# Kernel tuning notes

Measured on AMD Instinct MI355X. Metric: run time of the kernel, lower is better.

Reference implementation:

```python
import jax, jax.numpy as jnp
import numpy as np

D_MODEL = 1024
NUM_HEADS = 16
D_K = D_MODEL // NUM_HEADS
D_FF = 4096
B, S = 4, 2048
EPS = 1e-5


def _linear_params(key, d_in, d_out):
    # torch nn.Linear default init: U(-1/sqrt(d_in), 1/sqrt(d_in))
    k1, k2 = jax.random.split(key)
    bound = 1.0 / np.sqrt(d_in)
    W = jax.random.uniform(k1, (d_in, d_out), jnp.float32, -bound, bound)
    b = jax.random.uniform(k2, (d_out,), jnp.float32, -bound, bound)
    return W, b


def setup_inputs() -> dict:
    key = jax.random.key(0)
    ks = jax.random.split(key, 8)
    x = jax.random.normal(ks[0], (B, S, D_MODEL), jnp.float32)
    Wq, bq = _linear_params(ks[1], D_MODEL, D_MODEL)
    Wk, bk = _linear_params(ks[2], D_MODEL, D_MODEL)
    Wv, bv = _linear_params(ks[3], D_MODEL, D_MODEL)
    Wo, bo = _linear_params(ks[4], D_MODEL, D_MODEL)
    W1, b1 = _linear_params(ks[5], D_MODEL, D_FF)
    W2, b2 = _linear_params(ks[6], D_FF, D_MODEL)
    ln1_g = jnp.ones((D_MODEL,), jnp.float32)
    ln1_b = jnp.zeros((D_MODEL,), jnp.float32)
    ln2_g = jnp.ones((D_MODEL,), jnp.float32)
    ln2_b = jnp.zeros((D_MODEL,), jnp.float32)
    return dict(x=x, Wq=Wq, bq=bq, Wk=Wk, bk=bk, Wv=Wv, bv=bv, Wo=Wo, bo=bo,
                W1=W1, b1=b1, W2=W2, b2=b2,
                ln1_g=ln1_g, ln1_b=ln1_b, ln2_g=ln2_g, ln2_b=ln2_b)


def _layernorm(x, g, b):
    mu = jnp.mean(x, axis=-1, keepdims=True)
    var = jnp.mean(jnp.square(x - mu), axis=-1, keepdims=True)
    return (x - mu) * jax.lax.rsqrt(var + EPS) * g + b


def _attention(h, Wq, bq, Wk, bk, Wv, bv, Wo, bo):
    b, s, _ = h.shape
    def split_heads(t):  # (b,s,d) -> (b,H,s,dk)
        return t.reshape(b, s, NUM_HEADS, D_K).transpose(0, 2, 1, 3)
    Q = split_heads(h @ Wq + bq)
    K = split_heads(h @ Wk + bk)
    V = split_heads(h @ Wv + bv)
    scores = jnp.einsum('bhqd,bhkd->bhqk', Q, K) / np.sqrt(D_K)
    causal = jnp.tril(jnp.ones((s, s), dtype=bool))  # True = keep
    scores = jnp.where(causal, scores, -jnp.inf)
    attn = jax.nn.softmax(scores, axis=-1)
    out = jnp.einsum('bhqk,bhkd->bhqd', attn, V)
    out = out.transpose(0, 2, 1, 3).reshape(b, s, D_MODEL)
    return out @ Wo + bo


def reference(x, Wq, bq, Wk, bk, Wv, bv, Wo, bo, W1, b1, W2, b2,
              ln1_g, ln1_b, ln2_g, ln2_b):
    # pre-norm residual block
    x = x + _attention(_layernorm(x, ln1_g, ln1_b), Wq, bq, Wk, bk, Wv, bv, Wo, bo)
    h = _layernorm(x, ln2_g, ln2_b)
    x = x + (jax.nn.relu(h @ W1 + b1) @ W2 + b2)
    return x
```

## Files before the change

### kernel.cpp

```cpp
#include <hip/hip_runtime.h>
#include <hip/hip_bf16.h>

typedef __bf16 bf16;
typedef __attribute__((ext_vector_type(8))) __bf16 bf16x8;
typedef __attribute__((ext_vector_type(4))) float f32x4;

#define D_MODEL 1024
#define NHEADS  16
#define DK      64
#define DFF     4096
#define BATCH   4
#define SEQ     2048
#define NTOK    (BATCH*SEQ)
#define QSCALE  0.18033688011112042f

#if __has_builtin(__builtin_amdgcn_exp2f)
#define EXP2F(x) __builtin_amdgcn_exp2f(x)
#else
#define EXP2F(x) exp2f(x)
#endif

__device__ __forceinline__ void gload16(const bf16* g, bf16* l) {
    __builtin_amdgcn_global_load_lds((const __attribute__((address_space(1))) void*)g,
                                     (__attribute__((address_space(3))) void*)l, 16, 0, 0);
}

__global__ __launch_bounds__(256) void transpose_cast4(
    const float* __restrict__ W0, const float* __restrict__ W1,
    const float* __restrict__ W2, const float* __restrict__ W3,
    bf16* __restrict__ T0, bf16* __restrict__ T1,
    bf16* __restrict__ T2, bf16* __restrict__ T3)
{
    const int z = blockIdx.z;
    const float* W = (z == 0) ? W0 : (z == 1) ? W1 : (z == 2) ? W2 : W3;
    bf16*       Wt = (z == 0) ? T0 : (z == 1) ? T1 : (z == 2) ? T2 : T3;
    const int K = 1024, N = 1024;
    __shared__ float tile[32][33];
    const int tx = threadIdx.x, ty = threadIdx.y;
    const int n0 = blockIdx.x * 32, k0 = blockIdx.y * 32;
#pragma unroll
    for (int i = 0; i < 4; ++i)
        tile[ty + i*8][tx] = W[(size_t)(k0 + ty + i*8) * N + n0 + tx];
    __syncthreads();
#pragma unroll
    for (int i = 0; i < 4; ++i)
        Wt[(size_t)(n0 + ty + i*8) * K + k0 + tx] = (bf16)tile[tx][ty + i*8];
}

__global__ __launch_bounds__(256) void transpose_cast(
    const float* __restrict__ W, bf16* __restrict__ Wt, int K, int N)
{
    __shared__ float tile[32][33];
    const int tx = threadIdx.x, ty = threadIdx.y;
    const int n0 = blockIdx.x * 32, k0 = blockIdx.y * 32;
#pragma unroll
    for (int i = 0; i < 4; ++i)
        tile[ty + i*8][tx] = W[(size_t)(k0 + ty + i*8) * N + n0 + tx];
    __syncthreads();
#pragma unroll
    for (int i = 0; i < 4; ++i)
        Wt[(size_t)(n0 + ty + i*8) * K + k0 + tx] = (bf16)tile[tx][ty + i*8];
}

__global__ __launch_bounds__(256) void transpose_v(
    const bf16* __restrict__ V, bf16* __restrict__ VT)
{
    __shared__ bf16 t[64][72];
    const int bh = blockIdx.y;
    const int s0 = blockIdx.x * 64;
    const int r  = threadIdx.x >> 2;
    const int c0 = (threadIdx.x & 3) * 16;
    const bf16* Vb = V  + (size_t)bh * SEQ * DK;
    bf16*       Tb = VT + (size_t)bh * DK * SEQ;
#pragma unroll
    for (int i = 0; i < 2; ++i) {
        bf16x8 v = *(const bf16x8*)&Vb[(size_t)(s0 + r) * DK + c0 + i*8];
#pragma unroll
        for (int j = 0; j < 8; ++j) t[c0 + i*8 + j][r] = v[j];
    }
    __syncthreads();
#pragma unroll
    for (int i = 0; i < 2; ++i) {
        bf16x8 o;
#pragma unroll
        for (int j = 0; j < 8; ++j) o[j] = t[r][c0 + i*8 + j];
        *(bf16x8*)&Tb[(size_t)r * SEQ + s0 + c0 + i*8] = o;
    }
}

__global__ __launch_bounds__(256) void ln_kernel(
    const float* __restrict__ x, const float* __restrict__ g,
    const float* __restrict__ beta, bf16* __restrict__ out)
{
    const int row = blockIdx.x, tid = threadIdx.x;
    const f32x4* xr = (const f32x4*)(x + (size_t)row * D_MODEL);
    f32x4 v = xr[tid];
    float s  = v[0] + v[1] + v[2] + v[3];
    float s2 = v[0]*v[0] + v[1]*v[1] + v[2]*v[2] + v[3]*v[3];
#pragma unroll
    for (int off = 32; off > 0; off >>= 1) {
        s  += __shfl_down(s,  off, 64);
        s2 += __shfl_down(s2, off, 64);
    }
    __shared__ float red[8];
    const int wave = tid >> 6, lane = tid & 63;
    if (lane == 0) { red[wave] = s; red[wave + 4] = s2; }
    __syncthreads();
    if (tid == 0) {
        float a = red[0] + red[1] + red[2] + red[3];
        float c = red[4] + red[5] + red[6] + red[7];
        float mu  = a * (1.0f / D_MODEL);
        float var = c * (1.0f / D_MODEL) - mu * mu;
        red[0] = mu;
        red[1] = rsqrtf(var + 1e-5f);
    }
    __syncthreads();
    const float mu = red[0], rs = red[1];
    f32x4 gv = ((const f32x4*)g)[tid];
    f32x4 bv = ((const f32x4*)beta)[tid];
    union { bf16 h[4]; uint2 u; } o;
#pragma unroll
    for (int i = 0; i < 4; ++i) o.h[i] = (bf16)((v[i] - mu) * rs * gv[i] + bv[i]);
    *(uint2*)(out + (size_t)row * D_MODEL + tid * 4) = o.u;
}

#define PH_WAIT() do { \
    __builtin_amdgcn_s_barrier(); \
    asm volatile("s_waitcnt lgkmcnt(0)" ::: "memory"); \
    __builtin_amdgcn_sched_barrier(0); \
} while (0)

template<int EPI>
__global__ __launch_bounds__(512, 2) void gemm256(
    const bf16* __restrict__ A, const bf16* __restrict__ Bt,
    const float* __restrict__ bias, const float* __restrict__ bias2,
    const float* __restrict__ bias3, const float* __restrict__ resid,
    void* __restrict__ outp, int M, int N, int K)
{
    __shared__ __align__(16) bf16 smem[65536];
    const int tid  = threadIdx.x;
    const int wave = tid >> 6, lane = tid & 63;
    const int quad = lane >> 4, l16 = lane & 15;
    const int wr = wave >> 2, wcn = wave & 3;
    const int m0 = blockIdx.x * 256, n0 = blockIdx.y * 256;
    const int NT = K >> 6;

    const bf16* gA[2]; const bf16* gB[2]; int ldsOff[2];
#pragma unroll
    for (int l = 0; l < 2; ++l) {
        const int slot = tid + l * 512;
        const int r = slot >> 2;
        const int clog = (slot & 3) ^ ((r >> 1) & 3);
        gA[l] = A  + (size_t)(m0 + r) * K + clog * 8;
        gB[l] = Bt + (size_t)(n0 + r) * K + clog * 8;
        ldsOff[l] = (wave * 64 + l * 512) * 8;
    }

    auto stageA = [&](int buf, int t, int kk) {
        bf16* dst = smem + (buf * 2 + kk) * 8192;
#pragma unroll
        for (int l = 0; l < 2; ++l) gload16(gA[l] + t * 64 + kk * 32, dst + ldsOff[l]);
    };
    auto stageB = [&](int buf, int t, int kk) {
        bf16* dst = smem + 32768 + (buf * 2 + kk) * 8192;
#pragma unroll
        for (int l = 0; l < 2; ++l) gload16(gB[l] + t * 64 + kk * 32, dst + ldsOff[l]);
    };

    const int cswz  = (quad ^ ((l16 >> 1) & 3)) * 8;
    const int aBase = (wr * 128 + l16) * 32 + cswz;
    const int bBase = (wcn * 64 + l16) * 32 + cswz;

    f32x4 acc[8][4];
    const f32x4 vzero = {0.f, 0.f, 0.f, 0.f};
#pragma unroll
    for (int i = 0; i < 8; ++i)
#pragma unroll
        for (int j = 0; j < 4; ++j) acc[i][j] = vzero;

    stageA(0, 0, 0); stageB(0, 0, 0);
    stageA(0, 0, 1); stageB(0, 0, 1);
    if (NT > 1) {
        stageA(1, 1, 0); stageB(1, 1, 0);
        asm volatile("s_waitcnt vmcnt(4)" ::: "memory");
    } else {
        asm volatile("s_waitcnt vmcnt(0)" ::: "memory");
    }
    __builtin_amdgcn_s_barrier();

    bf16x8 af[4], bfr[4];
#define GMM_MFMA(mh) do { \
    __builtin_amdgcn_s_setprio(1); \
    _Pragma("unroll") \
    for (int i_ = 0; i_ < 4; ++i_) { \
        _Pragma("unroll") \
        for (int j_ = 0; j_ < 4; ++j_) \
            acc[(mh)*4 + i_][j_] = __builtin_amdgcn_mfma_f32_16x16x32_bf16(af[i_], bfr[j_], acc[(mh)*4 + i_][j_], 0, 0, 0); \
    } \
    __builtin_amdgcn_s_setprio(0); \
    __builtin_amdgcn_s_barrier(); \
} while (0)

#pragma unroll 1
    for (int t = 0; t < NT; ++t) {
        const int buf = t & 1;
        const bf16* As0 = smem + buf * 16384;
        const bf16* As1 = As0 + 8192;
        const bf16* Bs0 = smem + 32768 + buf * 16384;
        const bf16* Bs1 = Bs0 + 8192;

#pragma unroll
        for (int i = 0; i < 4; ++i) af[i]  = *(const bf16x8*)&As0[aBase + i * 512];
#pragma unroll
        for (int j = 0; j < 4; ++j) bfr[j] = *(const bf16x8*)&Bs0[bBase + j * 512];
        if (t + 1 < NT) stageA(buf ^ 1, t + 1, 1);
        PH_WAIT();
        GMM_MFMA(0);

#pragma unroll
        for (int i = 0; i < 4; ++i) af[i] = *(const bf16x8*)&As0[aBase + 2048 + i * 512];
        if (t + 1 < NT) stageB(buf ^ 1, t + 1, 1);
        PH_WAIT();
        GMM_MFMA(1);

#pragma unroll
        for (int i = 0; i < 4; ++i) af[i]  = *(const bf16x8*)&As1[aBase + 2048 + i * 512];
#pragma unroll
        for (int j = 0; j < 4; ++j) bfr[j] = *(const bf16x8*)&Bs1[bBase + j * 512];
        if (t + 2 < NT) stageA(buf, t + 2, 0);
        PH_WAIT();
        GMM_MFMA(1);

#pragma unroll
        for (int i = 0; i < 4; ++i) af[i] = *(const bf16x8*)&As1[aBase + i * 512];
        if (t + 2 < NT) {
            stageB(buf, t + 2, 0);
            asm volatile("s_waitcnt vmcnt(4)" ::: "memory");
        } else {
            asm volatile("s_waitcnt vmcnt(0)" ::: "memory");
        }
        PH_WAIT();
        GMM_MFMA(0);
    }
#undef GMM_MFMA

#pragma unroll
    for (int mf = 0; mf < 8; ++mf) {
#pragma unroll
        for (int nf = 0; nf < 4; ++nf) {
            const int col = n0 + wcn * 64 + nf * 16 + l16;
            float bcol, sc = 1.0f;
            if (EPI == 0) {
                const int seg = col >> 10;
                const float* bp = (seg == 0) ? bias : ((seg == 1) ? bias2 : bias3);
                bcol = bp[col & 1023];
                if (seg == 0) sc = QSCALE;
            } else {
                bcol = bias[col];
            }
#pragma unroll
            for (int r = 0; r < 4; ++r) {
                const int row = m0 + wr * 128 + mf * 16 + quad * 4 + r;
                const float v = acc[mf][nf][r] + bcol;
                if (EPI == 0) {
                    const int bb = row >> 11, ss = row & (SEQ - 1);
                    const int hh = (col & 1023) >> 6, dd = col & (DK - 1);
                    const size_t seg = (size_t)(col >> 10);
                    ((bf16*)outp)[seg * 8388608 + (((size_t)(bb * NHEADS + hh)) * SEQ + ss) * DK + dd] = (bf16)(v * sc);
                } else if (EPI == 1) {
                    const size_t idx = (size_t)row * N + col;
                    ((float*)outp)[idx] = v + resid[idx];
                } else {
                    ((bf16*)outp)[(size_t)row * N + col] = (bf16)fmaxf(v, 0.f);
                }
            }
        }
    }
}

template<int EPI>
__global__ __launch_bounds__(512, 2) void gemm256n128(
    const bf16* __restrict__ A, const bf16* __restrict__ Bt,
    const float* __restrict__ bias, const float* __restrict__ bias2,
    const float* __restrict__ bias3, const float* __restrict__ resid,
    void* __restrict__ outp, int M, int N, int K)
{
    __shared__ __align__(16) bf16 smem[49152];
    const int tid  = threadIdx.x;
    const int wave = tid >> 6, lane = tid & 63;
    const int quad = lane >> 4, l16 = lane & 15;
    const int wr = wave >> 1, wcn = wave & 1;
    const int m0 = blockIdx.x * 256, n0 = blockIdx.y * 128;
    const int NT = K >> 6;

    const bf16* gA[2]; const bf16* gB0; int ldsOffA[2];
#pragma unroll
    for (int l = 0; l < 2; ++l) {
        const int slot = tid + l * 512;
        const int r = slot >> 2;
        const int clog = (slot & 3) ^ ((r >> 1) & 3);
        gA[l] = A + (size_t)(m0 + r) * K + clog * 8;
        ldsOffA[l] = (wave * 64 + l * 512) * 8;
    }
    {
        const int r = tid >> 2;
        const int clog = (tid & 3) ^ ((r >> 1) & 3);
        gB0 = Bt + (size_t)(n0 + r) * K + clog * 8;
    }
    const int ldsOffB = wave * 512;

    auto stageA = [&](int buf, int t, int kk) {
        bf16* dst = smem + (buf * 2 + kk) * 8192;
#pragma unroll
        for (int l = 0; l < 2; ++l) gload16(gA[l] + t * 64 + kk * 32, dst + ldsOffA[l]);
    };
    auto stageB = [&](int buf, int t, int kk) {
        bf16* dst = smem + 32768 + (buf * 2 + kk) * 4096;
        gload16(gB0 + t * 64 + kk * 32, dst + ldsOffB);
    };

    const int cswz  = (quad ^ ((l16 >> 1) & 3)) * 8;
    const int aBase = (wr * 64 + l16) * 32 + cswz;
    const int bBase = (wcn * 64 + l16) * 32 + cswz;

    f32x4 acc[4][4];
    const f32x4 vzero = {0.f, 0.f, 0.f, 0.f};
#pragma unroll
    for (int i = 0; i < 4; ++i)
#pragma unroll
        for (int j = 0; j < 4; ++j) acc[i][j] = vzero;

    stageA(0, 0, 0); stageB(0, 0, 0);
    stageA(0, 0, 1); stageB(0, 0, 1);
    if (NT > 1) {
        stageA(1, 1, 0); stageB(1, 1, 0);
        asm volatile("s_waitcnt vmcnt(3)" ::: "memory");
    } else {
        asm volatile("s_waitcnt vmcnt(0)" ::: "memory");
    }
    __builtin_amdgcn_s_barrier();

    bf16x8 af[4], bfr[4];
#define GMM_MFMA16() do { \
    __builtin_amdgcn_s_setprio(1); \
    _Pragma("unroll") \
    for (int i_ = 0; i_ < 4; ++i_) { \
        _Pragma("unroll") \
        for (int j_ = 0; j_ < 4; ++j_) \
            acc[i_][j_] = __builtin_amdgcn_mfma_f32_16x16x32_bf16(af[i_], bfr[j_], acc[i_][j_], 0, 0, 0); \
    } \
    __builtin_amdgcn_s_setprio(0); \
    __builtin_amdgcn_s_barrier(); \
} while (0)

#pragma unroll 1
    for (int t = 0; t < NT; ++t) {
        const int buf = t & 1;
        const bf16* As0 = smem + buf * 16384;
        const bf16* As1 = As0 + 8192;
        const bf16* Bs0 = smem + 32768 + buf * 8192;
        const bf16* Bs1 = Bs0 + 4096;

#pragma unroll
        for (int i = 0; i < 4; ++i) af[i]  = *(const bf16x8*)&As0[aBase + i * 512];
#pragma unroll
        for (int j = 0; j < 4; ++j) bfr[j] = *(const bf16x8*)&Bs0[bBase + j * 512];
        if (t + 1 < NT) { stageA(buf ^ 1, t + 1, 1); stageB(buf ^ 1, t + 1, 1); }
        PH_WAIT();
        GMM_MFMA16();

#pragma unroll
        for (int i = 0; i < 4; ++i) af[i]  = *(const bf16x8*)&As1[aBase + i * 512];
#pragma unroll
        for (int j = 0; j < 4; ++j) bfr[j] = *(const bf16x8*)&Bs1[bBase + j * 512];
        if (t + 2 < NT) {
            stageA(buf, t + 2, 0); stageB(buf, t + 2, 0);
            asm volatile("s_waitcnt vmcnt(3)" ::: "memory");
        } else {
            asm volatile("s_waitcnt vmcnt(0)" ::: "memory");
        }
        PH_WAIT();
        GMM_MFMA16();
    }
#undef GMM_MFMA16

#pragma unroll
    for (int mf = 0; mf < 4; ++mf) {
#pragma unroll
        for (int nf = 0; nf < 4; ++nf) {
            const int col = n0 + wcn * 64 + nf * 16 + l16;
            float bcol, sc = 1.0f;
            if (EPI == 0) {
                const int seg = col >> 10;
                const float* bp = (seg == 0) ? bias : ((seg == 1) ? bias2 : bias3);
                bcol = bp[col & 1023];
                if (seg == 0) sc = QSCALE;
            } else {
                bcol = bias[col];
            }
#pragma unroll
            for (int r = 0; r < 4; ++r) {
                const int row = m0 + wr * 64 + mf * 16 + quad * 4 + r;
                const float v = acc[mf][nf][r] + bcol;
                if (EPI == 0) {
                    const int bb = row >> 11, ss = row & (SEQ - 1);
                    const int hh = (col & 1023) >> 6, dd = col & (DK - 1);
                    const size_t seg = (size_t)(col >> 10);
                    ((bf16*)outp)[seg * 8388608 + (((size_t)(bb * NHEADS + hh)) * SEQ + ss) * DK + dd] = (bf16)(v * sc);
                } else if (EPI == 1) {
                    const size_t idx = (size_t)row * N + col;
                    ((float*)outp)[idx] = v + resid[idx];
                } else {
                    ((bf16*)outp)[(size_t)row * N + col] = (bf16)fmaxf(v, 0.f);
                }
            }
        }
    }
}

__global__ __launch_bounds__(256, 2) void attn_kernel(
    const bf16* __restrict__ Q, const bf16* __restrict__ K,
    const bf16* __restrict__ VT, bf16* __restrict__ out)
{
    const int bh = blockIdx.x;
    const int b = bh >> 4, h = bh & 15;
    const int tid  = threadIdx.x;
    const int wave = tid >> 6, lane = tid & 63;
    const int quad = lane >> 4, l16 = lane & 15;

    __shared__ __align__(16) bf16 smem[32768 + 4 * 1152];
    bf16* Pw = smem + 32768 + wave * 1152;

    const bf16* Qb = Q  + (size_t)bh * SEQ * DK;
    const bf16* Kb = K  + (size_t)bh * SEQ * DK;
    const bf16* Vb = VT + (size_t)bh * DK * SEQ;

    int goK[4], goV[4], lo[4];
#pragma unroll
    for (int i = 0; i < 4; ++i) {
        const int U = (wave * 4 + i) * 64 + lane;
        const int rK = U >> 3, uK = (U & 7) ^ (rK & 7);
        goK[i] = rK * DK + uK * 8;
        const int rV = U >> 4, usw = U & 15;
        const int uV = (usw & 8) | ((usw & 7) ^ (rV & 7));
        goV[i] = rV * SEQ + uV * 8;
        lo[i]  = (wave * 4 + i) * 512;
    }

    auto stage = [&](int buf, int t) {
        const bf16* kp = Kb + (size_t)(t * 128) * DK;
        const bf16* vp = Vb + t * 128;
        bf16* kb = smem + buf * 8192;
        bf16* vb = smem + 16384 + buf * 8192;
#pragma unroll
        for (int i = 0; i < 4; ++i) gload16(kp + goK[i], kb + lo[i]);
#pragma unroll
        for (int i = 0; i < 4; ++i) gload16(vp + goV[i], vb + lo[i]);
    };

    const f32x4 vzero = {0.f, 0.f, 0.f, 0.f};
    int g = 0;
    stage(0, 0);

    for (int phase = 0; phase < 2; ++phase) {
        const int qt = phase ? (int)blockIdx.y : 15 - (int)blockIdx.y;
        const int qw = qt * 128 + wave * 32;

        bf16x8 qf[2][2];
#pragma unroll
        for (int qi = 0; qi < 2; ++qi)
#pragma unroll
            for (int kk = 0; kk < 2; ++kk)
                qf[qi][kk] = *(const bf16x8*)&Qb[(size_t)(qw + qi*16 + l16) * DK + kk*32 + quad*8];

        f32x4 Oacc[2][4];
        float m_[2], l_[2];
#pragma unroll
        for (int qi = 0; qi < 2; ++qi) {
            m_[qi] = -1.0e30f; l_[qi] = 0.f;
#pragma unroll
            for (int dj = 0; dj < 4; ++dj) Oacc[qi][dj] = vzero;
        }

        for (int t = 0; t <= qt; ++t, ++g) {
            const int cur = g & 1;
            __syncthreads();
            if (t < qt)            stage(cur ^ 1, t + 1);
            else if (phase == 0)   stage(cur ^ 1, 0);
            const bf16* kb = smem + cur * 8192;
            const bf16* vb = smem + 16384 + cur * 8192;
            const int kv0 = t * 128;

            f32x4 sv[8][2];
#pragma unroll
            for (int kvt = 0; kvt < 8; ++kvt) {
                const int R = kvt*16 + l16, rx = R & 7;
                bf16x8 kf0 = *(const bf16x8*)&kb[R*64 + (quad ^ rx)*8];
                bf16x8 kf1 = *(const bf16x8*)&kb[R*64 + (((quad + 4) & 7) ^ rx)*8];
                __builtin_amdgcn_s_setprio(1);
#pragma unroll
                for (int qi = 0; qi < 2; ++qi) {
                    f32x4 tacc = vzero;
                    tacc = __builtin_amdgcn_mfma_f32_16x16x32_bf16(kf0, qf[qi][0], tacc, 0, 0, 0);
                    tacc = __builtin_amdgcn_mfma_f32_16x16x32_bf16(kf1, qf[qi][1], tacc, 0, 0, 0);
                    sv[kvt][qi] = tacc;
                }
                __builtin_amdgcn_s_setprio(0);
            }

            if (t == qt) {
#pragma unroll
                for (int kvt = 0; kvt < 8; ++kvt)
#pragma unroll
                    for (int qi = 0; qi < 2; ++qi)
#pragma unroll
                        for (int r = 0; r < 4; ++r) {
                            const int kv = kv0 + kvt*16 + quad*4 + r;
                            const int q  = qw + qi*16 + l16;
                            if (kv > q) sv[kvt][qi][r] = -1.0e30f;
                        }
            }

            float mx[2];
#pragma unroll
            for (int qi = 0; qi < 2; ++qi) {
                float hx[8];
#pragma unroll
                for (int kvt = 0; kvt < 8; ++kvt)
                    hx[kvt] = fmaxf(fmaxf(fmaxf(sv[kvt][qi][0], sv[kvt][qi][1]), sv[kvt][qi][2]), sv[kvt][qi][3]);
                float m4 = fmaxf(fmaxf(fmaxf(hx[0], hx[1]), hx[2]), hx[3]);
                m4 = fmaxf(fmaxf(fmaxf(m4, hx[4]), fmaxf(hx[5], hx[6])), hx[7]);
                m4 = fmaxf(m4, __shfl_xor(m4, 16, 64));
                mx[qi] = fmaxf(m4, __shfl_xor(m4, 32, 64));
            }

            if (__any((mx[0] > m_[0] + 8.f) || (mx[1] > m_[1] + 8.f))) {
#pragma unroll
                for (int qi = 0; qi < 2; ++qi) {
                    const float newm  = fmaxf(m_[qi], mx[qi]);
                    const float alpha = EXP2F(m_[qi] - newm);
                    m_[qi] = newm;
                    l_[qi] *= alpha;
#pragma unroll
                    for (int dj = 0; dj < 4; ++dj) Oacc[qi][dj] *= alpha;
                }
            }

#pragma unroll
            for (int qi = 0; qi < 2; ++qi) {
                float rs = 0.f;
#pragma unroll
                for (int kvt = 0; kvt < 8; ++kvt)
#pragma unroll
                    for (int r = 0; r < 4; ++r) {
                        const float p = EXP2F(sv[kvt][qi][r] - m_[qi]);
                        sv[kvt][qi][r] = p;
                        rs += p;
                    }
                rs += __shfl_xor(rs, 16, 64);
                rs += __shfl_xor(rs, 32, 64);
                l_[qi] += rs;
            }

#pragma unroll
            for (int c2 = 0; c2 < 4; ++c2) {
                bf16x8 vf[4];
#pragma unroll
                for (int dj = 0; dj < 4; ++dj) {
                    const int R = dj*16 + l16;
                    const int u = c2*4 + quad;
                    const int usw = (u & 8) | ((u & 7) ^ (R & 7));
                    vf[dj] = *(const bf16x8*)&vb[R*128 + usw*8];
                }
#pragma unroll
                for (int qi = 0; qi < 2; ++qi) {
                    const f32x4 A = sv[c2*2 + 0][qi];
                    const f32x4 B = sv[c2*2 + 1][qi];
                    union { bf16 h[2]; int u; } pA01, pA23, pB01, pB23;
                    pA01.h[0] = (bf16)A[0]; pA01.h[1] = (bf16)A[1];
                    pA23.h[0] = (bf16)A[2]; pA23.h[1] = (bf16)A[3];
                    pB01.h[0] = (bf16)B[0]; pB01.h[1] = (bf16)B[1];
                    pB23.h[0] = (bf16)B[2]; pB23.h[1] = (bf16)B[3];
                    int a01 = pA01.u, a23 = pA23.u, b01 = pB01.u, b23 = pB23.u;
                    asm volatile("v_permlane32_swap_b32 %0, %1" : "+v"(a01), "+v"(b01));
                    asm volatile("v_permlane32_swap_b32 %0, %1" : "+v"(a23), "+v"(b23));
                    const int x01 = __shfl_xor(b01, 16, 64);
                    const int x23 = __shfl_xor(b23, 16, 64);
                    const int y01 = __shfl_xor(a01, 16, 64);
                    const int y23 = __shfl_xor(a23, 16, 64);
                    const bool odd = (quad & 1) != 0;
                    union { int w[4]; bf16x8 v; } pf;
                    pf.w[0] = odd ? x01 : a01;
                    pf.w[1] = odd ? x23 : a23;
                    pf.w[2] = odd ? b01 : y01;
                    pf.w[3] = odd ? b23 : y23;
                    __builtin_amdgcn_s_setprio(1);
#pragma unroll
                    for (int dj = 0; dj < 4; ++dj)
                        Oacc[qi][dj] = __builtin_amdgcn_mfma_f32_16x16x32_bf16(vf[dj], pf.v, Oacc[qi][dj], 0, 0, 0);
                    __builtin_amdgcn_s_setprio(0);
                }
            }
        }

        const float inv0 = 1.0f / l_[0], inv1 = 1.0f / l_[1];
#pragma unroll
        for (int dh = 0; dh < 2; ++dh) {
#pragma unroll
            for (int qi = 0; qi < 2; ++qi) {
                const float inv = qi ? inv1 : inv0;
#pragma unroll
                for (int djl = 0; djl < 2; ++djl) {
                    const int dj = dh*2 + djl;
                    union { bf16 h[4]; unsigned long long u; } ok;
#pragma unroll
                    for (int r = 0; r < 4; ++r) ok.h[r] = (bf16)(Oacc[qi][dj][r] * inv);
                    *(unsigned long long*)&Pw[(qi*16 + l16)*36 + djl*16 + quad*4] = ok.u;
                }
            }
            const int row = lane >> 1;
#pragma unroll
            for (int it = 0; it < 2; ++it) {
                const int grp = (lane & 1) + 2*it;
                bf16x8 o = *(const bf16x8*)&Pw[row*36 + grp*8];
                *(bf16x8*)&out[((size_t)(b*SEQ + qw - wave*32 + wave*32 + row))*D_MODEL + h*DK + dh*32 + grp*8] = o;
            }
        }
    }
}

extern "C" void kernel_launch(void* const* d_in, const int* in_sizes, int n_in,
                              void* d_out, int out_size, void* d_ws, size_t ws_size,
                              hipStream_t stream)
{
    const float* x    = (const float*)d_in[0];
    const float* Wq   = (const float*)d_in[1];
    const float* bq   = (const float*)d_in[2];
    const float* Wk   = (const float*)d_in[3];
    const float* bk   = (const float*)d_in[4];
    const float* Wv   = (const float*)d_in[5];
    const float* bv   = (const float*)d_in[6];
    const float* Wo   = (const float*)d_in[7];
    const float* bo   = (const float*)d_in[8];
    const float* W1   = (const float*)d_in[9];
    const float* b1   = (const float*)d_in[10];
    const float* W2   = (const float*)d_in[11];
    const float* b2   = (const float*)d_in[12];
    const float* ln1g = (const float*)d_in[13];
    const float* ln1b = (const float*)d_in[14];
    const float* ln2g = (const float*)d_in[15];
    const float* ln2b = (const float*)d_in[16];

    char* ws = (char*)d_ws;
    const size_t MB = 1024 * 1024;
    bf16* WTq  = (bf16*)(ws + 0 * MB);
    bf16* WTk  = (bf16*)(ws + 2 * MB);
    bf16* WTv  = (bf16*)(ws + 4 * MB);
    bf16* WTo  = (bf16*)(ws + 6 * MB);
    bf16* WT1  = (bf16*)(ws + 8 * MB);
    bf16* WT2  = (bf16*)(ws + 16 * MB);
    bf16* hbuf = (bf16*)(ws + 24 * MB);
    bf16* VhT  = (bf16*)(ws + 24 * MB);
    bf16* Qh   = (bf16*)(ws + 40 * MB);
    bf16* Kh   = (bf16*)(ws + 56 * MB);
    bf16* Vh   = (bf16*)(ws + 72 * MB);
    bf16* attn = (bf16*)(ws + 88 * MB);
    bf16* ff1  = (bf16*)(ws + 40 * MB);
    float* x2  = (float*)d_out;

    dim3 tb(32, 8);
    transpose_cast4<<<dim3(32, 32, 4), tb, 0, stream>>>(Wq, Wk, Wv, Wo, WTq, WTk, WTv, WTo);
    transpose_cast<<<dim3(128, 32), tb, 0, stream>>>(W1, WT1, 1024, 4096);
    transpose_cast<<<dim3(32, 128), tb, 0, stream>>>(W2, WT2, 4096, 1024);

    ln_kernel<<<NTOK, 256, 0, stream>>>(x, ln1g, ln1b, hbuf);

    gemm256n128<0><<<dim3(32, 24), 512, 0, stream>>>(hbuf, WTq, bq, bk, bv, nullptr, Qh, NTOK, 3072, 1024);

    transpose_v<<<dim3(32, 64), 256, 0, stream>>>(Vh, VhT);

    attn_kernel<<<dim3(64, 8), 256, 0, stream>>>(Qh, Kh, VhT, attn);

    gemm256n128<1><<<dim3(32, 8), 512, 0, stream>>>(attn, WTo, bo, nullptr, nullptr, x, x2, NTOK, 1024, 1024);

    ln_kernel<<<NTOK, 256, 0, stream>>>(x2, ln2g, ln2b, hbuf);

    gemm256<2><<<dim3(32, 16), 512, 0, stream>>>(hbuf, WT1, b1, nullptr, nullptr, nullptr, ff1, NTOK, 4096, 1024);
    gemm256n128<1><<<dim3(32, 8), 512, 0, stream>>>(ff1, WT2, b2, nullptr, nullptr, x2, x2, NTOK, 1024, 4096);
}
```

Baseline: 468.2 us.

## Split-K the FFN down-projection with 256x256 tiles and atomic accumulation

```diff
diff --git a/kernel.cpp b/kernel.cpp
--- a/kernel.cpp
+++ b/kernel.cpp
@@ -133,9 +133,8 @@
 template<int EPI>
 __global__ __launch_bounds__(512, 2) void gemm256(
     const bf16* __restrict__ A, const bf16* __restrict__ Bt,
-    const float* __restrict__ bias, const float* __restrict__ bias2,
-    const float* __restrict__ bias3, const float* __restrict__ resid,
-    void* __restrict__ outp, int M, int N, int K)
+    const float* __restrict__ bias,
+    void* __restrict__ outp, int M, int N, int K, int ldk)
 {
     __shared__ __align__(16) bf16 smem[65536];
     const int tid  = threadIdx.x;
@@ -144,6 +143,7 @@
     const int wr = wave >> 2, wcn = wave & 3;
     const int m0 = blockIdx.x * 256, n0 = blockIdx.y * 256;
     const int NT = K >> 6;
+    const int kOff = blockIdx.z * K;
 
     const bf16* gA[2]; const bf16* gB[2]; int ldsOff[2];
 #pragma unroll
@@ -151,8 +151,8 @@
         const int slot = tid + l * 512;
         const int r = slot >> 2;
         const int clog = (slot & 3) ^ ((r >> 1) & 3);
-        gA[l] = A  + (size_t)(m0 + r) * K + clog * 8;
-        gB[l] = Bt + (size_t)(n0 + r) * K + clog * 8;
+        gA[l] = A  + (size_t)(m0 + r) * ldk + kOff + clog * 8;
+        gB[l] = Bt + (size_t)(n0 + r) * ldk + kOff + clog * 8;
         ldsOff[l] = (wave * 64 + l * 512) * 8;
     }
 
@@ -249,29 +249,17 @@
 #pragma unroll
         for (int nf = 0; nf < 4; ++nf) {
             const int col = n0 + wcn * 64 + nf * 16 + l16;
-            float bcol, sc = 1.0f;
-            if (EPI == 0) {
-                const int seg = col >> 10;
-                const float* bp = (seg == 0) ? bias : ((seg == 1) ? bias2 : bias3);
-                bcol = bp[col & 1023];
-                if (seg == 0) sc = QSCALE;
-            } else {
-                bcol = bias[col];
-            }
+            float bcol;
+            if (EPI == 3) bcol = (blockIdx.z == 0) ? bias[col] : 0.f;
+            else          bcol = bias[col];
 #pragma unroll
             for (int r = 0; r < 4; ++r) {
                 const int row = m0 + wr * 128 + mf * 16 + quad * 4 + r;
                 const float v = acc[mf][nf][r] + bcol;
-                if (EPI == 0) {
-                    const int bb = row >> 11, ss = row & (SEQ - 1);
-                    const int hh = (col & 1023) >> 6, dd = col & (DK - 1);
-                    const size_t seg = (size_t)(col >> 10);
-                    ((bf16*)outp)[seg * 8388608 + (((size_t)(bb * NHEADS + hh)) * SEQ + ss) * DK + dd] = (bf16)(v * sc);
-                } else if (EPI == 1) {
-                    const size_t idx = (size_t)row * N + col;
-                    ((float*)outp)[idx] = v + resid[idx];
+                if (EPI == 2) {
+                    ((bf16*)outp)[(size_t)row * N + col] = (bf16)fmaxf(v, 0.f);
                 } else {
-                    ((bf16*)outp)[(size_t)row * N + col] = (bf16)fmaxf(v, 0.f);
+                    atomicAdd(&((float*)outp)[(size_t)row * N + col], v);
                 }
             }
         }
@@ -685,6 +673,6 @@
 
     ln_kernel<<<NTOK, 256, 0, stream>>>(x2, ln2g, ln2b, hbuf);
 
-    gemm256<2><<<dim3(32, 16), 512, 0, stream>>>(hbuf, WT1, b1, nullptr, nullptr, nullptr, ff1, NTOK, 4096, 1024);
-    gemm256n128<1><<<dim3(32, 8), 512, 0, stream>>>(ff1, WT2, b2, nullptr, nullptr, x2, x2, NTOK, 1024, 4096);
-}
+    gemm256<2><<<dim3(32, 16), 512, 0, stream>>>(hbuf, WT1, b1, ff1, NTOK, 4096, 1024, 1024);
+    gemm256<3><<<dim3(32, 4, 2), 512, 0, stream>>>(ff1, WT2, b2, x2, NTOK, 1024, 2048, 4096);
+}
```

After: 509.5 us. +8.8%, slower.

## Double-buffer GEMM register fragments to overlap LDS reads with MFMA

Applied to the files above, without the earlier changes.

```diff
diff --git a/kernel.cpp b/kernel.cpp
--- a/kernel.cpp
+++ b/kernel.cpp
@@ -340,49 +340,56 @@
     }
     __builtin_amdgcn_s_barrier();
 
-    bf16x8 af[4], bfr[4];
-#define GMM_MFMA16() do { \
+    bf16x8 af0[4], bf0[4], af1[4], bf1[4];
+#pragma unroll
+    for (int i = 0; i < 4; ++i) af0[i] = *(const bf16x8*)&smem[aBase + i * 512];
+#pragma unroll
+    for (int j = 0; j < 4; ++j) bf0[j] = *(const bf16x8*)&smem[32768 + bBase + j * 512];
+
+#define GMM_MFMA_N(AF, BF) do { \
     __builtin_amdgcn_s_setprio(1); \
     _Pragma("unroll") \
     for (int i_ = 0; i_ < 4; ++i_) { \
         _Pragma("unroll") \
         for (int j_ = 0; j_ < 4; ++j_) \
-            acc[i_][j_] = __builtin_amdgcn_mfma_f32_16x16x32_bf16(af[i_], bfr[j_], acc[i_][j_], 0, 0, 0); \
+            acc[i_][j_] = __builtin_amdgcn_mfma_f32_16x16x32_bf16(AF[i_], BF[j_], acc[i_][j_], 0, 0, 0); \
     } \
     __builtin_amdgcn_s_setprio(0); \
-    __builtin_amdgcn_s_barrier(); \
 } while (0)
 
 #pragma unroll 1
     for (int t = 0; t < NT; ++t) {
         const int buf = t & 1;
-        const bf16* As0 = smem + buf * 16384;
-        const bf16* As1 = As0 + 8192;
-        const bf16* Bs0 = smem + 32768 + buf * 8192;
-        const bf16* Bs1 = Bs0 + 4096;
-
-#pragma unroll
-        for (int i = 0; i < 4; ++i) af[i]  = *(const bf16x8*)&As0[aBase + i * 512];
-#pragma unroll
-        for (int j = 0; j < 4; ++j) bfr[j] = *(const bf16x8*)&Bs0[bBase + j * 512];
+        const bf16* As1  = smem + (buf * 2 + 1) * 8192;
+        const bf16* Bs1  = smem + 32768 + (buf * 2 + 1) * 4096;
+        const bf16* As0n = smem + ((buf ^ 1) * 2) * 8192;
+        const bf16* Bs0n = smem + 32768 + ((buf ^ 1) * 2) * 4096;
+
+#pragma unroll
+        for (int i = 0; i < 4; ++i) af1[i] = *(const bf16x8*)&As1[aBase + i * 512];
+#pragma unroll
+        for (int j = 0; j < 4; ++j) bf1[j] = *(const bf16x8*)&Bs1[bBase + j * 512];
         if (t + 1 < NT) { stageA(buf ^ 1, t + 1, 1); stageB(buf ^ 1, t + 1, 1); }
-        PH_WAIT();
-        GMM_MFMA16();
-
-#pragma unroll
-        for (int i = 0; i < 4; ++i) af[i]  = *(const bf16x8*)&As1[aBase + i * 512];
-#pragma unroll
-        for (int j = 0; j < 4; ++j) bfr[j] = *(const bf16x8*)&Bs1[bBase + j * 512];
-        if (t + 2 < NT) {
-            stageA(buf, t + 2, 0); stageB(buf, t + 2, 0);
-            asm volatile("s_waitcnt vmcnt(3)" ::: "memory");
-        } else {
-            asm volatile("s_waitcnt vmcnt(0)" ::: "memory");
+        __builtin_amdgcn_sched_barrier(0);
+        GMM_MFMA_N(af0, bf0);
+        if (t + 1 < NT) asm volatile("s_waitcnt vmcnt(3)" ::: "memory");
+        else            asm volatile("s_waitcnt vmcnt(0)" ::: "memory");
+        __builtin_amdgcn_s_barrier();
+
+        if (t + 1 < NT) {
+#pragma unroll
+            for (int i = 0; i < 4; ++i) af0[i] = *(const bf16x8*)&As0n[aBase + i * 512];
+#pragma unroll
+            for (int j = 0; j < 4; ++j) bf0[j] = *(const bf16x8*)&Bs0n[bBase + j * 512];
         }
-        PH_WAIT();
-        GMM_MFMA16();
-    }
-#undef GMM_MFMA16
+        if (t + 2 < NT) { stageA(buf, t + 2, 0); stageB(buf, t + 2, 0); }
+        __builtin_amdgcn_sched_barrier(0);
+        GMM_MFMA_N(af1, bf1);
+        if (t + 2 < NT) asm volatile("s_waitcnt vmcnt(3)" ::: "memory");
+        else            asm volatile("s_waitcnt vmcnt(0)" ::: "memory");
+        __builtin_amdgcn_s_barrier();
+    }
+#undef GMM_MFMA_N
 
 #pragma unroll
     for (int mf = 0; mf < 4; ++mf) {
```

After: 469.9 us. Within noise of the previous version (+0.4%).
